# Kernel optimization log

Measured on AMD Instinct MI355X. Metric: run time of the kernel, lower is better.

The kernel has to match this reference:

```python
import jax, jax.numpy as jnp
import numpy as np

B, N, D_MODEL, H, BLK = 2, 2048, 1024, 16, 128
TB = N // BLK  # 16 blocks per side
NEG = -1e30


def setup_inputs() -> dict:
    key = jax.random.key(0)
    kq, kk, kv, kb = jax.random.split(key, 4)
    q = jax.random.normal(kq, (B, N, D_MODEL), jnp.float32)
    k = jax.random.normal(kk, (B, N, D_MODEL), jnp.float32)
    v = jax.random.normal(kv, (B, N, D_MODEL), jnp.float32)
    tau = jnp.float32(1.0)
    mask = jnp.ones((B, 1, N, N), jnp.int32)
    block_sparse_mask = jax.random.randint(kb, (TB, TB), 0, 2).astype(jnp.int32)
    return {"q": q, "k": k, "v": v, "tau": tau, "mask": mask,
            "block_sparse_mask": block_sparse_mask}


def reference(q, k, v, tau, mask, block_sparse_mask):
    # Equivalent closed form of the tiled online-softmax loop (dropout p=0, eval
    # mode): processed blocks accumulate exactly masked softmax(tau*QK^T/sqrt(dk))@V;
    # rows whose every block is skipped keep O=0, l=0, m=-inf.
    Bq, Nq, D = q.shape
    d_k = D // H
    qh = q.reshape(Bq, Nq, H, d_k).transpose(0, 2, 1, 3)  # (B,H,N,dk)
    kh = k.reshape(Bq, Nq, H, d_k).transpose(0, 2, 1, 3)
    vh = v.reshape(Bq, Nq, H, d_k).transpose(0, 2, 1, 3)

    S = tau * jnp.einsum('bhqd,bhkd->bhqk', qh, kh) / np.sqrt(d_k).astype(np.float32)

    # expand block-sparse pattern to token resolution (N,N)
    bs = jnp.repeat(jnp.repeat(block_sparse_mask, BLK, axis=0), BLK, axis=1)
    allowed = (mask != 0) & (bs != 0)  # (B,1,N,N), broadcasts over heads

    S_m = jnp.where(allowed, S, NEG)
    m = jnp.max(S_m, axis=-1, keepdims=True)            # (B,H,N,1)
    P = jnp.exp(S_m - m) * allowed.astype(S.dtype)      # masked exp-weights
    l = jnp.sum(P, axis=-1, keepdims=True)              # (B,H,N,1)
    Ov = jnp.einsum('bhqk,bhkd->bhqd', P, vh)
    O = Ov / jnp.where(l > 0, l, 1.0)

    has_any = jnp.any(allowed, axis=-1, keepdims=True)  # (B,1,N,1)
    m_out = jnp.where(has_any, m, -jnp.inf)
    O_out = O.transpose(0, 2, 1, 3).reshape(Bq, Nq, D)
    return O_out, l, m_out
```

## Files before the change

kernel.cpp:

```cpp
#include <hip/hip_runtime.h>
#include <hip/hip_bf16.h>

#define B_   2
#define N_   2048
#define DM_  1024
#define H_   16
#define DK_  64
#define BLK_ 128
#define TB_  16

typedef unsigned short u16;
typedef unsigned int   u32;
using bf16x8 = __attribute__((ext_vector_type(8))) __bf16;
using f32x4  = __attribute__((ext_vector_type(4))) float;

#define KPAD 72
#define VPAD 136
#define PPAD 136
#define OPAD 68

__device__ __forceinline__ u32 pack_bf16(float a, float b) {
  __hip_bfloat162 h = __float22bfloat162_rn(make_float2(a, b));
  u32 u; __builtin_memcpy(&u, &h, 4); return u;
}
__device__ __forceinline__ bf16x8 pack8(float4 f0, float4 f1, float sc) {
  u32 w[4];
  w[0] = pack_bf16(f0.x * sc, f0.y * sc); w[1] = pack_bf16(f0.z * sc, f0.w * sc);
  w[2] = pack_bf16(f1.x * sc, f1.y * sc); w[3] = pack_bf16(f1.z * sc, f1.w * sc);
  bf16x8 r; __builtin_memcpy(&r, w, 16); return r;
}

__global__ void kv_convert(const float* __restrict__ k, const float* __restrict__ v,
                           u16* __restrict__ kb, u16* __restrict__ vt) {
  __shared__ u16 tile[BLK_][DK_ + 2];
  const int b = blockIdx.z, h = blockIdx.y, nb = blockIdx.x;
  const int t = threadIdx.x;
  const int rr = t >> 4, cc = (t & 15) * 4;
  {
    const float* kg = k + ((size_t)(b * N_ + nb * BLK_)) * DM_ + h * DK_;
    u16* kd = kb + ((size_t)((b * H_ + h) * N_) + nb * BLK_) * DK_;
#pragma unroll
    for (int i = 0; i < 8; ++i) {
      const int r = rr + i * 16;
      const float4 f = *(const float4*)(kg + (size_t)r * DM_ + cc);
      *(uint2*)(kd + r * DK_ + cc) = make_uint2(pack_bf16(f.x, f.y), pack_bf16(f.z, f.w));
    }
  }
  {
    const float* vg = v + ((size_t)(b * N_ + nb * BLK_)) * DM_ + h * DK_;
#pragma unroll
    for (int i = 0; i < 8; ++i) {
      const int r = rr + i * 16;
      const float4 f = *(const float4*)(vg + (size_t)r * DM_ + cc);
      *(u32*)(&tile[r][cc])     = pack_bf16(f.x, f.y);
      *(u32*)(&tile[r][cc + 2]) = pack_bf16(f.z, f.w);
    }
    __syncthreads();
    const int d = t >> 2, n0 = (t & 3) * 32;
    u16* og = vt + ((size_t)(b * H_ + h) * DK_ + d) * N_ + nb * BLK_ + n0;
#pragma unroll
    for (int j = 0; j < 32; j += 8) {
      u16 tmp[8];
#pragma unroll
      for (int x = 0; x < 8; ++x) tmp[x] = tile[n0 + j + x][d];
      uint4 w; __builtin_memcpy(&w, tmp, 16);
      *(uint4*)(og + j) = w;
    }
  }
}

__global__ void mask_flags_kernel(const int* __restrict__ mask, const int* __restrict__ bs,
                                  int* __restrict__ flags) {
  const int blk = blockIdx.x;
  const int kb = blk % TB_, qb = (blk / TB_) % TB_, b = blk / (TB_ * TB_);
  const int t = threadIdx.x;
  const int* mg = mask + (size_t)b * N_ * N_ + (size_t)(qb * BLK_) * N_ + kb * BLK_;
  int all1 = 1, any1 = 0;
  for (int i = t; i < BLK_ * BLK_ / 4; i += 256) {
    const int r = i >> 5, c = (i & 31) * 4;
    const int4 mv = *(const int4*)(mg + (size_t)r * N_ + c);
    all1 &= (mv.x != 0) & (mv.y != 0) & (mv.z != 0) & (mv.w != 0);
    any1 |= (mv.x != 0) | (mv.y != 0) | (mv.z != 0) | (mv.w != 0);
  }
  __shared__ int sAll[4], sAny[4];
  const int wv = t >> 6;
  const int wAll = __all(all1), wAny = __any(any1);
  if ((t & 63) == 0) { sAll[wv] = wAll; sAny[wv] = wAny; }
  __syncthreads();
  if (t == 0) {
    const int A = sAll[0] & sAll[1] & sAll[2] & sAll[3];
    const int O = sAny[0] | sAny[1] | sAny[2] | sAny[3];
    int f = 0;
    if (bs[qb * TB_ + kb] != 0 && O) f = A ? 1 : 2;
    flags[blk] = f;
  }
}

__global__ __launch_bounds__(256, 2)
void attn_kernel(const float* __restrict__ q_, const u16* __restrict__ kb_,
                 const u16* __restrict__ vt, const float* __restrict__ tau_p,
                 const int* __restrict__ mask, const int* __restrict__ flags,
                 float* __restrict__ o_out, float* __restrict__ l_out,
                 float* __restrict__ m_out) {
  __shared__ __align__(16) u16 lds[BLK_ * KPAD + DK_ * VPAD + BLK_ * PPAD];
  u16* Ks  = lds;
  u16* Vts = Ks + BLK_ * KPAD;
  u16* Ps  = Vts + DK_ * VPAD;
  float* Os = (float*)lds;

  const int idx = blockIdx.x;
  const int bh = idx & 31, qb128 = idx >> 5;
  const int b = bh >> 4, h = bh & 15;
  const int t = threadIdx.x;
  const int wave = t >> 6, lane = t & 63, quad = lane >> 4, col = lane & 15;

  const int* flg = flags + (b * TB_ + qb128) * TB_;
  u32 actmask = 0, mixmask = 0;
#pragma unroll
  for (int i = 0; i < TB_; ++i) {
    const int f = flg[i];
    actmask |= (f != 0) ? (1u << i) : 0u;
    mixmask |= (f == 2) ? (1u << i) : 0u;
  }

  int qg[2];
  qg[0] = qb128 * BLK_ + wave * 32 + col;
  qg[1] = qg[0] + 16;

  const float qscale = tau_p[0] * 0.125f * 1.44269504f;
  bf16x8 bq[2][2];
#pragma unroll
  for (int nt = 0; nt < 2; ++nt) {
    const float* qr = q_ + ((size_t)(b * N_ + qg[nt])) * DM_ + h * DK_;
#pragma unroll
    for (int half = 0; half < 2; ++half) {
      const float4 f0 = *(const float4*)(qr + half * 32 + quad * 8);
      const float4 f1 = *(const float4*)(qr + half * 32 + quad * 8 + 4);
      bq[nt][half] = pack8(f0, f1, qscale);
    }
  }

  float m_run[2] = {-INFINITY, -INFINITY};
  float l_run[2] = {0.f, 0.f};
  f32x4 oacc[2][4];
#pragma unroll
  for (int nt = 0; nt < 2; ++nt)
#pragma unroll
    for (int mt = 0; mt < 4; ++mt) oacc[nt][mt] = (f32x4){0.f, 0.f, 0.f, 0.f};

  const u16* kbase = kb_ + (size_t)(b * H_ + h) * N_ * DK_;
  const u16* vbase = vt + (size_t)(b * H_ + h) * DK_ * N_;

  u32 rem = actmask;
  while (rem) {
    const int cur = (int)__builtin_ctz(rem);
    rem &= rem - 1;
    const int mix = (mixmask >> cur) & 1;

    __syncthreads();
    {
      const u16* ks = kbase + (size_t)cur * BLK_ * DK_;
      const u16* vs = vbase + cur * BLK_;
      uint4 kr[4], vr[4];
#pragma unroll
      for (int j = 0; j < 4; ++j) {
        const int i = t + 256 * j;
        kr[j] = *(const uint4*)(ks + i * 8);
        vr[j] = *(const uint4*)(vs + (size_t)(i >> 4) * N_ + (i & 15) * 8);
      }
#pragma unroll
      for (int j = 0; j < 4; ++j) {
        const int i = t + 256 * j;
        *(uint4*)(Ks + (i >> 3) * KPAD + (i & 7) * 8) = kr[j];
        *(uint4*)(Vts + (i >> 4) * VPAD + (i & 15) * 8) = vr[j];
      }
    }
    __syncthreads();

#pragma unroll
    for (int nt = 0; nt < 2; ++nt) {
      f32x4 st[8];
#pragma unroll
      for (int kt = 0; kt < 8; ++kt) {
        const bf16x8 a0 = *(const bf16x8*)(Ks + (kt * 16 + col) * KPAD + quad * 8);
        const bf16x8 a1 = *(const bf16x8*)(Ks + (kt * 16 + col) * KPAD + 32 + quad * 8);
        f32x4 c = (f32x4){0.f, 0.f, 0.f, 0.f};
        c = __builtin_amdgcn_mfma_f32_16x16x32_bf16(a0, bq[nt][0], c, 0, 0, 0);
        c = __builtin_amdgcn_mfma_f32_16x16x32_bf16(a1, bq[nt][1], c, 0, 0, 0);
        st[kt] = c;
      }
      if (mix) {
        const int* mg = mask + (size_t)b * N_ * N_ + (size_t)qg[nt] * N_ + cur * BLK_;
#pragma unroll
        for (int kt = 0; kt < 8; ++kt) {
          const int4 mv = *(const int4*)(mg + kt * 16 + quad * 4);
          if (!mv.x) st[kt][0] = -1e30f;
          if (!mv.y) st[kt][1] = -1e30f;
          if (!mv.z) st[kt][2] = -1e30f;
          if (!mv.w) st[kt][3] = -1e30f;
        }
      }
      float mx = -INFINITY;
#pragma unroll
      for (int kt = 0; kt < 8; ++kt)
        mx = fmaxf(mx, fmaxf(fmaxf(st[kt][0], st[kt][1]), fmaxf(st[kt][2], st[kt][3])));
      mx = fmaxf(mx, __shfl_xor(mx, 16, 64));
      mx = fmaxf(mx, __shfl_xor(mx, 32, 64));
      const float mnew = fmaxf(m_run[nt], mx);
      const float alpha = __builtin_amdgcn_exp2f(m_run[nt] - mnew);
      const int qloc = wave * 32 + nt * 16 + col;
      float s = 0.f;
      if (!mix) {
#pragma unroll
        for (int kt = 0; kt < 8; ++kt) {
          const float p0 = __builtin_amdgcn_exp2f(st[kt][0] - mnew);
          const float p1 = __builtin_amdgcn_exp2f(st[kt][1] - mnew);
          const float p2 = __builtin_amdgcn_exp2f(st[kt][2] - mnew);
          const float p3 = __builtin_amdgcn_exp2f(st[kt][3] - mnew);
          s += (p0 + p1) + (p2 + p3);
          *(uint2*)(Ps + qloc * PPAD + kt * 16 + quad * 4) =
              make_uint2(pack_bf16(p0, p1), pack_bf16(p2, p3));
        }
      } else {
#pragma unroll
        for (int kt = 0; kt < 8; ++kt) {
          const float p0 = st[kt][0] <= -1e29f ? 0.f : __builtin_amdgcn_exp2f(st[kt][0] - mnew);
          const float p1 = st[kt][1] <= -1e29f ? 0.f : __builtin_amdgcn_exp2f(st[kt][1] - mnew);
          const float p2 = st[kt][2] <= -1e29f ? 0.f : __builtin_amdgcn_exp2f(st[kt][2] - mnew);
          const float p3 = st[kt][3] <= -1e29f ? 0.f : __builtin_amdgcn_exp2f(st[kt][3] - mnew);
          s += (p0 + p1) + (p2 + p3);
          *(uint2*)(Ps + qloc * PPAD + kt * 16 + quad * 4) =
              make_uint2(pack_bf16(p0, p1), pack_bf16(p2, p3));
        }
      }
      s += __shfl_xor(s, 16, 64);
      s += __shfl_xor(s, 32, 64);
      l_run[nt] = alpha * l_run[nt] + s;
      m_run[nt] = mnew;
#pragma unroll
      for (int mt = 0; mt < 4; ++mt)
#pragma unroll
        for (int r = 0; r < 4; ++r) oacc[nt][mt][r] *= alpha;
    }

#pragma unroll
    for (int ks = 0; ks < 4; ++ks) {
      bf16x8 bfrag[2];
#pragma unroll
      for (int nt = 0; nt < 2; ++nt)
        bfrag[nt] = *(const bf16x8*)(Ps + (wave * 32 + nt * 16 + col) * PPAD + ks * 32 + quad * 8);
#pragma unroll
      for (int mt = 0; mt < 4; ++mt) {
        const bf16x8 av = *(const bf16x8*)(Vts + (mt * 16 + col) * VPAD + ks * 32 + quad * 8);
#pragma unroll
        for (int nt = 0; nt < 2; ++nt)
          oacc[nt][mt] = __builtin_amdgcn_mfma_f32_16x16x32_bf16(av, bfrag[nt], oacc[nt][mt], 0, 0, 0);
      }
    }
  }

  __syncthreads();
#pragma unroll
  for (int nt = 0; nt < 2; ++nt) {
    const float inv = l_run[nt] > 0.f ? 1.f / l_run[nt] : 1.f;
    const int qloc = wave * 32 + nt * 16 + col;
#pragma unroll
    for (int mt = 0; mt < 4; ++mt) {
      float4 w = make_float4(oacc[nt][mt][0] * inv, oacc[nt][mt][1] * inv,
                             oacc[nt][mt][2] * inv, oacc[nt][mt][3] * inv);
      *(float4*)(Os + qloc * OPAD + mt * 16 + quad * 4) = w;
    }
  }
  __syncthreads();
  float* ob = o_out + ((size_t)(b * N_ + qb128 * BLK_)) * DM_ + h * DK_;
#pragma unroll
  for (int j = 0; j < 8; ++j) {
    const int i = t + 256 * j;
    const int r = i >> 4, c4 = (i & 15) * 4;
    const float4 w = *(const float4*)(Os + r * OPAD + c4);
    *(float4*)(ob + (size_t)r * DM_ + c4) = w;
  }
  if (quad == 0) {
#pragma unroll
    for (int nt = 0; nt < 2; ++nt) {
      const size_t oi = (size_t)(b * H_ + h) * N_ + qg[nt];
      l_out[oi] = l_run[nt];
      m_out[oi] = l_run[nt] > 0.f ? m_run[nt] * 0.69314718056f : -INFINITY;
    }
  }
}

extern "C" void kernel_launch(void* const* d_in, const int* in_sizes, int n_in,
                              void* d_out, int out_size, void* d_ws, size_t ws_size,
                              hipStream_t stream) {
  const float* q   = (const float*)d_in[0];
  const float* k   = (const float*)d_in[1];
  const float* v   = (const float*)d_in[2];
  const float* tau = (const float*)d_in[3];
  const int* mask  = (const int*)d_in[4];
  const int* bs    = (const int*)d_in[5];
  float* out = (float*)d_out;

  const size_t plane = (size_t)B_ * H_ * N_ * DK_;
  u16* kb = (u16*)d_ws;
  u16* vt = kb + plane;
  int* flags = (int*)(vt + plane);

  kv_convert<<<dim3(N_ / BLK_, H_, B_), 256, 0, stream>>>(k, v, kb, vt);
  mask_flags_kernel<<<B_ * TB_ * TB_, 256, 0, stream>>>(mask, bs, flags);

  float* o_out = out;
  float* l_out = out + (size_t)B_ * N_ * DM_;
  float* m_out = l_out + (size_t)B_ * H_ * N_;
  attn_kernel<<<dim3(TB_ * 32), 256, 0, stream>>>(q, kb, vt, tau, mask, flags,
                                                  o_out, l_out, m_out);
}
```

Before: 168.2 us.

## Prefetch next K/V block, lazy rescale softmax, reorder QK MFMA, set wave priority

Global loads for the next active key block are issued into registers before the current block is computed, so memory latency overlaps with MFMA and softmax work. The online softmax now rescales the accumulator only when the new row max exceeds the running max by more than a threshold, and tracks the true max separately to correct l and m at output. The QK^T loop is reordered to reuse K fragments across both query subtiles, s_setprio raises wave priority around the MFMA sections, and the V transpose thread mapping is changed. The prefetch adds register pressure, and the lazy rescale lets unnormalised values grow by up to 2^8 before rescaling.

```diff
diff --git a/kernel.cpp b/kernel.cpp
--- a/kernel.cpp
+++ b/kernel.cpp
@@ -56,7 +56,7 @@
       *(u32*)(&tile[r][cc + 2]) = pack_bf16(f.z, f.w);
     }
     __syncthreads();
-    const int d = t >> 2, n0 = (t & 3) * 32;
+    const int d = t & 63, n0 = (t >> 6) * 32;
     u16* og = vt + ((size_t)(b * H_ + h) * DK_ + d) * N_ + nb * BLK_ + n0;
 #pragma unroll
     for (int j = 0; j < 32; j += 8) {
@@ -123,6 +123,25 @@
     mixmask |= (f == 2) ? (1u << i) : 0u;
   }
 
+  const u16* kbase = kb_ + (size_t)(b * H_ + h) * N_ * DK_;
+  const u16* vbase = vt + (size_t)(b * H_ + h) * DK_ * N_;
+
+  uint4 kr[4], vr[4];
+  auto issue = [&](int blk) {
+    const u16* ks = kbase + (size_t)blk * BLK_ * DK_;
+    const u16* vs = vbase + blk * BLK_;
+#pragma unroll
+    for (int j = 0; j < 4; ++j) {
+      const int i = t + 256 * j;
+      kr[j] = *(const uint4*)(ks + i * 8);
+      vr[j] = *(const uint4*)(vs + (size_t)(i >> 4) * N_ + (i & 15) * 8);
+    }
+  };
+
+  u32 rem = actmask;
+  int cur = -1;
+  if (rem) { cur = (int)__builtin_ctz(rem); rem &= rem - 1; issue(cur); }
+
   int qg[2];
   qg[0] = qb128 * BLK_ + wave * 32 + col;
   qg[1] = qg[0] + 16;
@@ -140,7 +159,8 @@
     }
   }
 
-  float m_run[2] = {-INFINITY, -INFINITY};
+  float m_run[2]  = {-INFINITY, -INFINITY};
+  float m_true[2] = {-INFINITY, -INFINITY};
   float l_run[2] = {0.f, 0.f};
   f32x4 oacc[2][4];
 #pragma unroll
@@ -148,75 +168,81 @@
 #pragma unroll
     for (int mt = 0; mt < 4; ++mt) oacc[nt][mt] = (f32x4){0.f, 0.f, 0.f, 0.f};
 
-  const u16* kbase = kb_ + (size_t)(b * H_ + h) * N_ * DK_;
-  const u16* vbase = vt + (size_t)(b * H_ + h) * DK_ * N_;
-
-  u32 rem = actmask;
-  while (rem) {
-    const int cur = (int)__builtin_ctz(rem);
-    rem &= rem - 1;
+  while (cur >= 0) {
     const int mix = (mixmask >> cur) & 1;
 
     __syncthreads();
-    {
-      const u16* ks = kbase + (size_t)cur * BLK_ * DK_;
-      const u16* vs = vbase + cur * BLK_;
-      uint4 kr[4], vr[4];
-#pragma unroll
-      for (int j = 0; j < 4; ++j) {
-        const int i = t + 256 * j;
-        kr[j] = *(const uint4*)(ks + i * 8);
-        vr[j] = *(const uint4*)(vs + (size_t)(i >> 4) * N_ + (i & 15) * 8);
-      }
-#pragma unroll
-      for (int j = 0; j < 4; ++j) {
-        const int i = t + 256 * j;
-        *(uint4*)(Ks + (i >> 3) * KPAD + (i & 7) * 8) = kr[j];
-        *(uint4*)(Vts + (i >> 4) * VPAD + (i & 15) * 8) = vr[j];
-      }
+#pragma unroll
+    for (int j = 0; j < 4; ++j) {
+      const int i = t + 256 * j;
+      *(uint4*)(Ks + (i >> 3) * KPAD + (i & 7) * 8) = kr[j];
+      *(uint4*)(Vts + (i >> 4) * VPAD + (i & 15) * 8) = vr[j];
     }
     __syncthreads();
 
-#pragma unroll
-    for (int nt = 0; nt < 2; ++nt) {
-      f32x4 st[8];
-#pragma unroll
-      for (int kt = 0; kt < 8; ++kt) {
-        const bf16x8 a0 = *(const bf16x8*)(Ks + (kt * 16 + col) * KPAD + quad * 8);
-        const bf16x8 a1 = *(const bf16x8*)(Ks + (kt * 16 + col) * KPAD + 32 + quad * 8);
+    int nxt = -1;
+    if (rem) { nxt = (int)__builtin_ctz(rem); rem &= rem - 1; issue(nxt); }
+
+    f32x4 st[2][8];
+    __builtin_amdgcn_s_setprio(1);
+#pragma unroll
+    for (int kt = 0; kt < 8; ++kt) {
+      const bf16x8 a0 = *(const bf16x8*)(Ks + (kt * 16 + col) * KPAD + quad * 8);
+      const bf16x8 a1 = *(const bf16x8*)(Ks + (kt * 16 + col) * KPAD + 32 + quad * 8);
+#pragma unroll
+      for (int nt = 0; nt < 2; ++nt) {
         f32x4 c = (f32x4){0.f, 0.f, 0.f, 0.f};
         c = __builtin_amdgcn_mfma_f32_16x16x32_bf16(a0, bq[nt][0], c, 0, 0, 0);
         c = __builtin_amdgcn_mfma_f32_16x16x32_bf16(a1, bq[nt][1], c, 0, 0, 0);
-        st[kt] = c;
-      }
+        st[nt][kt] = c;
+      }
+    }
+    __builtin_amdgcn_s_setprio(0);
+
+#pragma unroll
+    for (int nt = 0; nt < 2; ++nt) {
       if (mix) {
         const int* mg = mask + (size_t)b * N_ * N_ + (size_t)qg[nt] * N_ + cur * BLK_;
 #pragma unroll
         for (int kt = 0; kt < 8; ++kt) {
           const int4 mv = *(const int4*)(mg + kt * 16 + quad * 4);
-          if (!mv.x) st[kt][0] = -1e30f;
-          if (!mv.y) st[kt][1] = -1e30f;
-          if (!mv.z) st[kt][2] = -1e30f;
-          if (!mv.w) st[kt][3] = -1e30f;
+          if (!mv.x) st[nt][kt][0] = -1e30f;
+          if (!mv.y) st[nt][kt][1] = -1e30f;
+          if (!mv.z) st[nt][kt][2] = -1e30f;
+          if (!mv.w) st[nt][kt][3] = -1e30f;
         }
       }
       float mx = -INFINITY;
 #pragma unroll
       for (int kt = 0; kt < 8; ++kt)
-        mx = fmaxf(mx, fmaxf(fmaxf(st[kt][0], st[kt][1]), fmaxf(st[kt][2], st[kt][3])));
+        mx = fmaxf(mx, fmaxf(fmaxf(st[nt][kt][0], st[nt][kt][1]),
+                             fmaxf(st[nt][kt][2], st[nt][kt][3])));
       mx = fmaxf(mx, __shfl_xor(mx, 16, 64));
       mx = fmaxf(mx, __shfl_xor(mx, 32, 64));
-      const float mnew = fmaxf(m_run[nt], mx);
-      const float alpha = __builtin_amdgcn_exp2f(m_run[nt] - mnew);
+      m_true[nt] = fmaxf(m_true[nt], mx);
+
+      const float mold = m_run[nt];
+      float mnew = mold;
+      if (!__all(mx <= mold + 8.f)) {
+        mnew = fmaxf(mold, mx);
+        const float alpha = __builtin_amdgcn_exp2f(mold - mnew);
+        l_run[nt] *= alpha;
+#pragma unroll
+        for (int mt = 0; mt < 4; ++mt)
+#pragma unroll
+          for (int r = 0; r < 4; ++r) oacc[nt][mt][r] *= alpha;
+        m_run[nt] = mnew;
+      }
+
       const int qloc = wave * 32 + nt * 16 + col;
       float s = 0.f;
       if (!mix) {
 #pragma unroll
         for (int kt = 0; kt < 8; ++kt) {
-          const float p0 = __builtin_amdgcn_exp2f(st[kt][0] - mnew);
-          const float p1 = __builtin_amdgcn_exp2f(st[kt][1] - mnew);
-          const float p2 = __builtin_amdgcn_exp2f(st[kt][2] - mnew);
-          const float p3 = __builtin_amdgcn_exp2f(st[kt][3] - mnew);
+          const float p0 = __builtin_amdgcn_exp2f(st[nt][kt][0] - mnew);
+          const float p1 = __builtin_amdgcn_exp2f(st[nt][kt][1] - mnew);
+          const float p2 = __builtin_amdgcn_exp2f(st[nt][kt][2] - mnew);
+          const float p3 = __builtin_amdgcn_exp2f(st[nt][kt][3] - mnew);
           s += (p0 + p1) + (p2 + p3);
           *(uint2*)(Ps + qloc * PPAD + kt * 16 + quad * 4) =
               make_uint2(pack_bf16(p0, p1), pack_bf16(p2, p3));
@@ -224,10 +250,10 @@
       } else {
 #pragma unroll
         for (int kt = 0; kt < 8; ++kt) {
-          const float p0 = st[kt][0] <= -1e29f ? 0.f : __builtin_amdgcn_exp2f(st[kt][0] - mnew);
-          const float p1 = st[kt][1] <= -1e29f ? 0.f : __builtin_amdgcn_exp2f(st[kt][1] - mnew);
-          const float p2 = st[kt][2] <= -1e29f ? 0.f : __builtin_amdgcn_exp2f(st[kt][2] - mnew);
-          const float p3 = st[kt][3] <= -1e29f ? 0.f : __builtin_amdgcn_exp2f(st[kt][3] - mnew);
+          const float p0 = st[nt][kt][0] <= -1e29f ? 0.f : __builtin_amdgcn_exp2f(st[nt][kt][0] - mnew);
+          const float p1 = st[nt][kt][1] <= -1e29f ? 0.f : __builtin_amdgcn_exp2f(st[nt][kt][1] - mnew);
+          const float p2 = st[nt][kt][2] <= -1e29f ? 0.f : __builtin_amdgcn_exp2f(st[nt][kt][2] - mnew);
+          const float p3 = st[nt][kt][3] <= -1e29f ? 0.f : __builtin_amdgcn_exp2f(st[nt][kt][3] - mnew);
           s += (p0 + p1) + (p2 + p3);
           *(uint2*)(Ps + qloc * PPAD + kt * 16 + quad * 4) =
               make_uint2(pack_bf16(p0, p1), pack_bf16(p2, p3));
@@ -235,14 +261,10 @@
       }
       s += __shfl_xor(s, 16, 64);
       s += __shfl_xor(s, 32, 64);
-      l_run[nt] = alpha * l_run[nt] + s;
-      m_run[nt] = mnew;
-#pragma unroll
-      for (int mt = 0; mt < 4; ++mt)
-#pragma unroll
-        for (int r = 0; r < 4; ++r) oacc[nt][mt][r] *= alpha;
-    }
-
+      l_run[nt] += s;
+    }
+
+    __builtin_amdgcn_s_setprio(1);
 #pragma unroll
     for (int ks = 0; ks < 4; ++ks) {
       bf16x8 bfrag[2];
@@ -257,6 +279,8 @@
           oacc[nt][mt] = __builtin_amdgcn_mfma_f32_16x16x32_bf16(av, bfrag[nt], oacc[nt][mt], 0, 0, 0);
       }
     }
+    __builtin_amdgcn_s_setprio(0);
+    cur = nxt;
   }
 
   __syncthreads();
@@ -284,8 +308,10 @@
 #pragma unroll
     for (int nt = 0; nt < 2; ++nt) {
       const size_t oi = (size_t)(b * H_ + h) * N_ + qg[nt];
-      l_out[oi] = l_run[nt];
-      m_out[oi] = l_run[nt] > 0.f ? m_run[nt] * 0.69314718056f : -INFINITY;
+      const float lv = l_run[nt] > 0.f
+          ? l_run[nt] * __builtin_amdgcn_exp2f(m_run[nt] - m_true[nt]) : 0.f;
+      l_out[oi] = lv;
+      m_out[oi] = l_run[nt] > 0.f ? m_true[nt] * 0.69314718056f : -INFINITY;
     }
   }
 }
```

New measurement: 191.1 us. +13.7%, slower.
